# Kernel tuning notes

Measured on AMD Instinct MI355X. Metric: run time of the kernel, lower is better.

The kernel has to match this reference:

```python
import jax, jax.numpy as jnp
import numpy as np

DIM = 2048
BATCH = 16384
NUM_LAYERS = 4
S_E, S_C, S_N = 0.1, 0.1, 0.05  # strength_entail/contra/neutral
DIV_CONST = 0.38                # divergence_from_alignment offset
NORM_CAP = 10.0

def _normalize(x, axis=-1, eps=1e-12):
    # torch F.normalize: x / max(||x||, eps)
    n = jnp.linalg.norm(x, axis=axis, keepdims=True)
    return x / jnp.maximum(n, eps)

def setup_inputs() -> dict:
    key = jax.random.key(0)
    ks = jax.random.split(key, 8)
    scale = 1.0 / np.sqrt(DIM)  # nn.Linear-like init scale
    return {
        "h0": jax.random.normal(ks[0], (BATCH, DIM), dtype=jnp.float32),
        "anchor_entail": jax.random.normal(ks[1], (DIM,), dtype=jnp.float32),
        "anchor_contra": jax.random.normal(ks[2], (DIM,), dtype=jnp.float32),
        "anchor_neutral": jax.random.normal(ks[3], (DIM,), dtype=jnp.float32),
        "W1": jax.random.normal(ks[4], (DIM, DIM), dtype=jnp.float32) * scale,
        "b1": jnp.zeros((DIM,), dtype=jnp.float32),
        "W2": jax.random.normal(ks[5], (DIM, DIM), dtype=jnp.float32) * scale,
        "b2": jnp.zeros((DIM,), dtype=jnp.float32),
    }

def reference(h0, anchor_entail, anchor_contra, anchor_neutral, W1, b1, W2, b2):
    h = h0
    e_dir = _normalize(anchor_entail, axis=0)
    c_dir = _normalize(anchor_contra, axis=0)
    n_dir = _normalize(anchor_neutral, axis=0)
    for _ in range(NUM_LAYERS):
        h_n = _normalize(h)                     # [B, D]
        a_e = h_n @ e_dir                       # [B]
        a_c = h_n @ c_dir
        a_n = h_n @ n_dir
        d_e = DIV_CONST - a_e
        d_c = DIV_CONST - a_c
        d_n = DIV_CONST - a_n
        delta = jnp.tanh(h @ W1.T + b1) @ W2.T + b2  # Linear-Tanh-Linear
        e_vec = _normalize(h - e_dir)
        c_vec = _normalize(h - c_dir)
        n_vec = _normalize(h - n_dir)
        h = (h + delta
             - S_E * d_e[:, None] * e_vec
             - S_C * d_c[:, None] * c_vec
             - S_N * d_n[:, None] * n_vec)
        h_norm = jnp.linalg.norm(h, axis=-1, keepdims=True)
        h = jnp.where(h_norm > NORM_CAP, h * (NORM_CAP / (h_norm + 1e-8)), h)
    return h
```

## Files before the change

### kernel.cpp

```cpp
#include <hip/hip_runtime.h>
#include <stdint.h>

#define DIM      2048
#define BATCH    16384
#define S_E      0.1f
#define S_C      0.1f
#define S_N      0.05f
#define DIVC     0.38f
#define NCAP     10.0f

typedef __attribute__((ext_vector_type(4))) float floatx4;
typedef __attribute__((ext_vector_type(8))) short short8;
typedef __attribute__((ext_vector_type(4))) short short4v;

__device__ __forceinline__ float bf2f(unsigned short u) {
  union { float f; unsigned v; } x; x.v = ((unsigned)u) << 16; return x.f;
}
__device__ __forceinline__ unsigned short f2bf(float f) {
  union { float f; unsigned v; } x; x.f = f;
  unsigned r = x.v + 0x7FFFu + ((x.v >> 16) & 1u);
  return (unsigned short)(r >> 16);
}

__device__ __forceinline__ void gload_lds16(const void* g, void* l) {
  __builtin_amdgcn_global_load_lds((const __attribute__((address_space(1))) void*)g,
                                   (__attribute__((address_space(3))) void*)l,
                                   16, 0, 0);
}

__global__ void k_detect(const unsigned short* __restrict__ h0u, int* __restrict__ flag) {
  const int lane = threadIdx.x;
  int bad = 0;
#pragma unroll
  for (int i = 0; i < 32; ++i) {
    const unsigned u = h0u[lane + i * 64];
    const unsigned e = (u >> 7) & 0xFF;
    bad |= (e >= 0x84);
  }
  const unsigned long long m = __ballot(bad);
  if (lane == 0) *flag = (m != 0ull) ? 1 : 0;
}

__global__ __launch_bounds__(256) void k_prep_w(
    const void* __restrict__ w1r, const void* __restrict__ w2r,
    const int* __restrict__ flag,
    unsigned short* __restrict__ W1b, unsigned short* __restrict__ W2b) {
  const void* src = blockIdx.y ? w2r : w1r;
  unsigned short* dst = blockIdx.y ? W2b : W1b;
  const long i4 = (long)blockIdx.x * 256 + threadIdx.x;
  if (*flag) {
    const float4 v = ((const float4*)src)[i4];
    short4v o;
    o.x = (short)f2bf(v.x); o.y = (short)f2bf(v.y);
    o.z = (short)f2bf(v.z); o.w = (short)f2bf(v.w);
    ((short4v*)dst)[i4] = o;
  } else {
    ((short4v*)dst)[i4] = ((const short4v*)src)[i4];
  }
}

__global__ __launch_bounds__(256) void k_prep_small(
    const void* __restrict__ b1r, const void* __restrict__ b2r,
    const void* __restrict__ a0r, const void* __restrict__ a1r,
    const void* __restrict__ a2r, const int* __restrict__ flag,
    float* __restrict__ b1f, float* __restrict__ b2f, float* __restrict__ dirs) {
  __shared__ float red[4];
  const int tid = threadIdx.x, wave = tid >> 6, lane = tid & 63;
  const int isf32 = *flag;
#pragma unroll
  for (int i = 0; i < 8; ++i) {
    const int idx = i * 256 + tid;
    b1f[idx] = isf32 ? ((const float*)b1r)[idx] : bf2f(((const unsigned short*)b1r)[idx]);
    b2f[idx] = isf32 ? ((const float*)b2r)[idx] : bf2f(((const unsigned short*)b2r)[idx]);
  }
  const void* ar[3] = { a0r, a1r, a2r };
  for (int a = 0; a < 3; ++a) {
    float v[8]; float s = 0.f;
#pragma unroll
    for (int i = 0; i < 8; ++i) {
      const int idx = i * 256 + tid;
      v[i] = isf32 ? ((const float*)ar[a])[idx] : bf2f(((const unsigned short*)ar[a])[idx]);
      s = fmaf(v[i], v[i], s);
    }
#pragma unroll
    for (int off = 32; off >= 1; off >>= 1) s += __shfl_xor(s, off);
    if (lane == 0) red[wave] = s;
    __syncthreads();
    const float S = red[0] + red[1] + red[2] + red[3];
    const float inv = 1.f / fmaxf(sqrtf(S), 1e-12f);
#pragma unroll
    for (int i = 0; i < 8; ++i) dirs[a * DIM + i * 256 + tid] = v[i] * inv;
    __syncthreads();
  }
}

__device__ __forceinline__ float4 row_coef(float S0, float Se, float Sc, float Sn) {
  const float Li = 1.f / fmaxf(sqrtf(S0), 1e-12f);
  const float ce = S_E * (DIVC - Se * Li) / fmaxf(sqrtf(fmaxf(S0 - 2.f * Se + 1.f, 0.f)), 1e-12f);
  const float cc = S_C * (DIVC - Sc * Li) / fmaxf(sqrtf(fmaxf(S0 - 2.f * Sc + 1.f, 0.f)), 1e-12f);
  const float cn = S_N * (DIVC - Sn * Li) / fmaxf(sqrtf(fmaxf(S0 - 2.f * Sn + 1.f, 0.f)), 1e-12f);
  float4 c; c.x = 1.f - (ce + cc + cn); c.y = ce; c.z = cc; c.w = cn; return c;
}

template<int FULL>
__global__ __launch_bounds__(256) void k_boot(
    const void* __restrict__ h0raw, const int* __restrict__ flag,
    const float* __restrict__ dirs, float* __restrict__ hf,
    unsigned short* __restrict__ hb, float4* __restrict__ coef,
    float* __restrict__ scl) {
  __shared__ float red[16];
  const long row = blockIdx.x;
  const int tid = threadIdx.x, wave = tid >> 6, lane = tid & 63;
  const int isf32 = *flag;
  float h[8];
  float s0 = 0.f, se = 0.f, sc = 0.f, sn = 0.f;
#pragma unroll
  for (int i = 0; i < 2; ++i) {
    const int c4 = i * 256 + tid;
    float4 hv;
    if (isf32) {
      hv = ((const float4*)h0raw + row * (DIM/4))[c4];
    } else {
      const short4v hs = ((const short4v*)h0raw + row * (DIM/4))[c4];
      hv.x = bf2f((unsigned short)hs.x); hv.y = bf2f((unsigned short)hs.y);
      hv.z = bf2f((unsigned short)hs.z); hv.w = bf2f((unsigned short)hs.w);
    }
    const float4 ev = ((const float4*)dirs)[c4];
    const float4 cv = ((const float4*)(dirs + DIM))[c4];
    const float4 nv = ((const float4*)(dirs + 2*DIM))[c4];
    h[i*4+0]=hv.x; h[i*4+1]=hv.y; h[i*4+2]=hv.z; h[i*4+3]=hv.w;
    s0 = fmaf(hv.x,hv.x,fmaf(hv.y,hv.y,fmaf(hv.z,hv.z,fmaf(hv.w,hv.w,s0))));
    se = fmaf(hv.x,ev.x,fmaf(hv.y,ev.y,fmaf(hv.z,ev.z,fmaf(hv.w,ev.w,se))));
    sc = fmaf(hv.x,cv.x,fmaf(hv.y,cv.y,fmaf(hv.z,cv.z,fmaf(hv.w,cv.w,sc))));
    sn = fmaf(hv.x,nv.x,fmaf(hv.y,nv.y,fmaf(hv.z,nv.z,fmaf(hv.w,nv.w,sn))));
  }
#pragma unroll
  for (int off = 32; off >= 1; off >>= 1) {
    s0 += __shfl_xor(s0, off); se += __shfl_xor(se, off);
    sc += __shfl_xor(sc, off); sn += __shfl_xor(sn, off);
  }
  if (lane == 0) { red[wave*4+0]=s0; red[wave*4+1]=se; red[wave*4+2]=sc; red[wave*4+3]=sn; }
  __syncthreads();
  if (tid == 0) {
    const float S0 = red[0]+red[4]+red[8]+red[12];
    const float Se = red[1]+red[5]+red[9]+red[13];
    const float Sc = red[2]+red[6]+red[10]+red[14];
    const float Sn = red[3]+red[7]+red[11]+red[15];
    coef[row] = row_coef(S0, Se, Sc, Sn);
    scl[row] = 1.f;
  }
#pragma unroll
  for (int i = 0; i < 2; ++i) {
    const int c4 = i * 256 + tid;
    if (FULL) {
      float4 o; o.x=h[i*4+0]; o.y=h[i*4+1]; o.z=h[i*4+2]; o.w=h[i*4+3];
      ((float4*)hf + row * (DIM/4))[c4] = o;
    }
    short4v ob;
    ob.x=(short)f2bf(h[i*4+0]); ob.y=(short)f2bf(h[i*4+1]);
    ob.z=(short)f2bf(h[i*4+2]); ob.w=(short)f2bf(h[i*4+3]);
    ((short4v*)hb + row * (DIM/4))[c4] = ob;
  }
}


template<int VM, bool STG>
__device__ __forceinline__ void gemm_tile(
    const int t, const unsigned short* __restrict__ Ag,
    const unsigned short* __restrict__ Bg, char* __restrict__ smem,
    const int tid, const int wm, const int wn, const int l16, const int quad,
    floatx4 (&acc)[8][4], short8 (&bfr)[4]) {
  const int qs = (quad ^ ((l16 >> 1) & 3)) * 8;
  const short* As = (const short*)(smem + (t & 3) * 32768) + (wm + l16) * 32 + qs;
  const short* Bs = (const short*)(smem + (t & 3) * 32768 + 16384) + (wn + l16) * 32 + qs;
  short8 af[4];
#pragma unroll
  for (int j = 0; j < 4; ++j) bfr[j] = *(const short8*)(Bs + j * 512);
#pragma unroll
  for (int i = 0; i < 4; ++i) af[i] = *(const short8*)(As + i * 512);
  if (STG) {
    const unsigned short* as = Ag + (t + 3) * 32;
    char* dA = smem + ((t + 3) & 3) * 32768 + tid * 16;
    gload_lds16(as, dA);
    gload_lds16(as + (size_t)128 * DIM, dA + 8192);
  }
  __builtin_amdgcn_s_barrier();
  __builtin_amdgcn_sched_barrier(0);
  __builtin_amdgcn_s_setprio(1);
#pragma unroll
  for (int i = 0; i < 4; ++i)
#pragma unroll
    for (int j = 0; j < 4; ++j)
      acc[i][j] = __builtin_amdgcn_mfma_f32_16x16x32_bf16(af[i], bfr[j], acc[i][j], 0, 0, 0);
  __builtin_amdgcn_s_setprio(0);
  __builtin_amdgcn_s_barrier();
  __builtin_amdgcn_sched_barrier(0);
#pragma unroll
  for (int i = 0; i < 4; ++i) af[i] = *(const short8*)(As + (4 + i) * 512);
  if (STG) {
    const unsigned short* bs = Bg + (t + 3) * 32;
    char* dB = smem + ((t + 3) & 3) * 32768 + 16384 + tid * 16;
    gload_lds16(bs, dB);
    gload_lds16(bs + (size_t)128 * DIM, dB + 8192);
  }
  __builtin_amdgcn_s_barrier();
  __builtin_amdgcn_sched_barrier(0);
  __builtin_amdgcn_s_setprio(1);
#pragma unroll
  for (int i = 0; i < 4; ++i)
#pragma unroll
    for (int j = 0; j < 4; ++j)
      acc[4 + i][j] = __builtin_amdgcn_mfma_f32_16x16x32_bf16(af[i], bfr[j], acc[4 + i][j], 0, 0, 0);
  __builtin_amdgcn_s_setprio(0);
  __builtin_amdgcn_sched_barrier(0);
  if constexpr (VM == 8)      asm volatile("s_waitcnt vmcnt(8)" ::: "memory");
  else if constexpr (VM == 4) asm volatile("s_waitcnt vmcnt(4)" ::: "memory");
  else if constexpr (VM == 0) asm volatile("s_waitcnt vmcnt(0)" ::: "memory");
  __builtin_amdgcn_s_barrier();
  __builtin_amdgcn_sched_barrier(0);
}

__device__ __forceinline__ void gemm_main(
    const unsigned short* __restrict__ A, const unsigned short* __restrict__ B,
    char* __restrict__ smem, const int tid, const int wm, const int wn,
    const int l16, const int quad, const long m0, const long n0,
    floatx4 (&acc)[8][4]) {
  const int csw = ((tid & 3) ^ ((tid >> 3) & 3)) * 8;
  const unsigned short* Ag = A + (m0 + (tid >> 2)) * DIM + csw;
  const unsigned short* Bg = B + (n0 + (tid >> 2)) * DIM + csw;
#pragma unroll
  for (int tt = 0; tt < 3; ++tt) {
    const unsigned short* as = Ag + tt * 32;
    const unsigned short* bs = Bg + tt * 32;
    char* dA = smem + tt * 32768 + tid * 16;
    char* dB = dA + 16384;
    gload_lds16(as, dA);
    gload_lds16(as + (size_t)128 * DIM, dA + 8192);
    gload_lds16(bs, dB);
    gload_lds16(bs + (size_t)128 * DIM, dB + 8192);
  }
  asm volatile("s_waitcnt vmcnt(8)" ::: "memory");
  __builtin_amdgcn_s_barrier();
  __builtin_amdgcn_sched_barrier(0);
  short8 bfr[4];
#pragma unroll 1
  for (int t = 0; t < DIM / 32 - 3; ++t)
    gemm_tile<8, true >(t, Ag, Bg, smem, tid, wm, wn, l16, quad, acc, bfr);
  gemm_tile<4, false>(DIM / 32 - 3, Ag, Bg, smem, tid, wm, wn, l16, quad, acc, bfr);
  gemm_tile<0, false>(DIM / 32 - 2, Ag, Bg, smem, tid, wm, wn, l16, quad, acc, bfr);
  gemm_tile<-1, false>(DIM / 32 - 1, Ag, Bg, smem, tid, wm, wn, l16, quad, acc, bfr);
}

__device__ __forceinline__ void xcd_tiles(long& m0, long& n0) {
  const int b = blockIdx.y * (DIM / 256) + blockIdx.x;
  const int swz = (b & 7) * ((BATCH / 256) * (DIM / 256) / 8) + (b >> 3);
  m0 = (long)(swz >> 3) * 256;
  n0 = (long)(swz & 7) * 256;
}

__global__ __launch_bounds__(512, 2) void gemm_tanh(
    const unsigned short* __restrict__ A, const unsigned short* __restrict__ B,
    const float* __restrict__ bias, const float* __restrict__ scl,
    unsigned short* __restrict__ Cb) {
  __shared__ __align__(16) char smem[131072];
  const int tid = threadIdx.x, wave = tid >> 6, lane = tid & 63;
  const int quad = lane >> 4, l16 = lane & 15;
  const int wm = (wave >> 2) * 128, wn = (wave & 3) * 64;
  long m0, n0;
  xcd_tiles(m0, n0);
  floatx4 acc[8][4] = {};
  gemm_main(A, B, smem, tid, wm, wn, l16, quad, m0, n0, acc);
  __syncthreads();
  asm volatile("" ::: "memory");
  short* Eh = (short*)smem;
  float sr[32];
#pragma unroll
  for (int i = 0; i < 8; ++i) {
    const float4 s4 = *(const float4*)(scl + m0 + wm + i * 16 + quad * 4);
    sr[i*4+0] = s4.x; sr[i*4+1] = s4.y; sr[i*4+2] = s4.z; sr[i*4+3] = s4.w;
  }
  float bcol[4];
#pragma unroll
  for (int j = 0; j < 4; ++j) bcol[j] = bias[n0 + wn + j * 16 + l16];
#pragma unroll
  for (int i = 0; i < 8; ++i) {
    const int row = wm + i * 16 + quad * 4;
#pragma unroll
    for (int j = 0; j < 4; ++j) {
      const int col = wn + j * 16 + l16;
#pragma unroll
      for (int r = 0; r < 4; ++r) {
        const float x = fmaf(sr[i*4+r], acc[i][j][r], bcol[j]);
        const float tt = 1.f - 2.f / (__expf(2.f * x) + 1.f);
        Eh[(row + r) * 256 + col] = (short)f2bf(tt);
      }
    }
  }
  __syncthreads();
#pragma unroll
  for (int s = 0; s < 16; ++s) {
    const int g = s * 512 + tid;
    const int row = g >> 5, c8 = (g & 31) * 8;
    *(short8*)(Cb + (m0 + row) * DIM + n0 + c8) = *(const short8*)(Eh + row * 256 + c8);
  }
}

template<int FULL>
__global__ __launch_bounds__(512, 2) void gemm_update(
    const unsigned short* __restrict__ A, const unsigned short* __restrict__ B,
    const float* __restrict__ bias, float* __restrict__ hf,
    unsigned short* __restrict__ hb, const float4* __restrict__ coef,
    const float* __restrict__ dirs) {
  __shared__ __align__(16) char smem[131072];
  const int tid = threadIdx.x, wave = tid >> 6, lane = tid & 63;
  const int quad = lane >> 4, l16 = lane & 15;
  const int wm = (wave >> 2) * 128, wn = (wave & 3) * 64;
  long m0, n0;
  xcd_tiles(m0, n0);
  floatx4 acc[8][4] = {};
  gemm_main(A, B, smem, tid, wm, wn, l16, quad, m0, n0, acc);
  asm volatile("" ::: "memory");
  float* Ef = (float*)smem;
#pragma unroll
  for (int p = 0; p < 2; ++p) {
    __syncthreads();
#pragma unroll
    for (int i = 0; i < 8; ++i) {
      const int row = wm + i * 16 + quad * 4;
#pragma unroll
      for (int jj = 0; jj < 2; ++jj) {
        const int cc = (wn >> 1) + jj * 16 + l16;
#pragma unroll
        for (int r = 0; r < 4; ++r)
          Ef[(row + r) * 128 + cc] = acc[i][p * 2 + jj][r];
      }
    }
    __syncthreads();
#pragma unroll
    for (int s = 0; s < 16; ++s) {
      const int q = s * 512 + tid;
      const int row = q >> 5, c4 = (q & 31) * 4;
      const int col = ((c4 >> 5) * 64) + p * 32 + (c4 & 31);
      const long gr = m0 + row, gc = n0 + col;
      const float4 e  = *(const float4*)(Ef + row * 128 + c4);
      const float4 bv = *(const float4*)(bias + gc);
      const float4 de = *(const float4*)(dirs + gc);
      const float4 dc = *(const float4*)(dirs + DIM + gc);
      const float4 dn = *(const float4*)(dirs + 2*DIM + gc);
      const float4 cf = coef[gr];
      float4 hv;
      if (FULL) {
        hv = *(const float4*)(hf + gr * DIM + gc);
      } else {
        const short4v hs = *(const short4v*)(hb + gr * DIM + gc);
        hv.x = bf2f((unsigned short)hs.x); hv.y = bf2f((unsigned short)hs.y);
        hv.z = bf2f((unsigned short)hs.z); hv.w = bf2f((unsigned short)hs.w);
      }
      float4 v;
      v.x = e.x + bv.x; v.y = e.y + bv.y; v.z = e.z + bv.z; v.w = e.w + bv.w;
      v.x = fmaf(cf.x, hv.x, v.x); v.y = fmaf(cf.x, hv.y, v.y);
      v.z = fmaf(cf.x, hv.z, v.z); v.w = fmaf(cf.x, hv.w, v.w);
      v.x = fmaf(cf.y, de.x, v.x); v.y = fmaf(cf.y, de.y, v.y);
      v.z = fmaf(cf.y, de.z, v.z); v.w = fmaf(cf.y, de.w, v.w);
      v.x = fmaf(cf.z, dc.x, v.x); v.y = fmaf(cf.z, dc.y, v.y);
      v.z = fmaf(cf.z, dc.z, v.z); v.w = fmaf(cf.z, dc.w, v.w);
      v.x = fmaf(cf.w, dn.x, v.x); v.y = fmaf(cf.w, dn.y, v.y);
      v.z = fmaf(cf.w, dn.z, v.z); v.w = fmaf(cf.w, dn.w, v.w);
      if (FULL) *(float4*)(hf + gr * DIM + gc) = v;
      short4v ob;
      ob.x = (short)f2bf(v.x); ob.y = (short)f2bf(v.y);
      ob.z = (short)f2bf(v.z); ob.w = (short)f2bf(v.w);
      *(short4v*)(hb + gr * DIM + gc) = ob;
    }
  }
}

__global__ __launch_bounds__(256) void k_stats(
    const unsigned short* __restrict__ hb, const float* __restrict__ dirs,
    float4* __restrict__ coef, float* __restrict__ scl) {
  const int tid = threadIdx.x, w = tid >> 6, lane = tid & 63;
  const long row = (long)blockIdx.x * 4 + w;
  const unsigned short* hr = hb + row * DIM;
  float s0 = 0.f, se = 0.f, sc = 0.f, sn = 0.f;
#pragma unroll
  for (int i = 0; i < 4; ++i) {
    const int o = i * 512 + lane * 8;
    const short8 h8 = *(const short8*)(hr + o);
    float h[8];
#pragma unroll
    for (int q = 0; q < 8; ++q) h[q] = bf2f((unsigned short)h8[q]);
    const float4 e0 = *(const float4*)(dirs + o),       e1 = *(const float4*)(dirs + o + 4);
    const float4 c0 = *(const float4*)(dirs + DIM + o), c1 = *(const float4*)(dirs + DIM + o + 4);
    const float4 n0v = *(const float4*)(dirs + 2*DIM + o), n1 = *(const float4*)(dirs + 2*DIM + o + 4);
    const float ee[8] = { e0.x,e0.y,e0.z,e0.w, e1.x,e1.y,e1.z,e1.w };
    const float ccv[8] = { c0.x,c0.y,c0.z,c0.w, c1.x,c1.y,c1.z,c1.w };
    const float nn[8] = { n0v.x,n0v.y,n0v.z,n0v.w, n1.x,n1.y,n1.z,n1.w };
#pragma unroll
    for (int q = 0; q < 8; ++q) {
      s0 = fmaf(h[q], h[q], s0);
      se = fmaf(h[q], ee[q], se);
      sc = fmaf(h[q], ccv[q], sc);
      sn = fmaf(h[q], nn[q], sn);
    }
  }
#pragma unroll
  for (int off = 32; off >= 1; off >>= 1) {
    s0 += __shfl_xor(s0, off); se += __shfl_xor(se, off);
    sc += __shfl_xor(sc, off); sn += __shfl_xor(sn, off);
  }
  if (lane == 0) {
    const float nrm = sqrtf(s0);
    const float s = (nrm > NCAP) ? (NCAP / (nrm + 1e-8f)) : 1.f;
    float4 cf = row_coef(s0 * s * s, se * s, sc * s, sn * s);
    cf.x *= s;
    coef[row] = cf;
    scl[row] = s;
  }
}

template<int FULL>
__global__ __launch_bounds__(256) void k_finish(
    const float* __restrict__ hf, const unsigned short* __restrict__ hb,
    const int* __restrict__ flag, void* __restrict__ dout) {
  const int tid = threadIdx.x, w = tid >> 6, lane = tid & 63;
  const long row = (long)blockIdx.x * 4 + w;
  float4 hv[8];
  float s0 = 0.f;
#pragma unroll
  for (int i = 0; i < 8; ++i) {
    const int o = i * 256 + lane * 4;
    if (FULL) {
      hv[i] = *(const float4*)(hf + row * DIM + o);
    } else {
      const short4v hs = *(const short4v*)(hb + row * DIM + o);
      hv[i].x = bf2f((unsigned short)hs.x); hv[i].y = bf2f((unsigned short)hs.y);
      hv[i].z = bf2f((unsigned short)hs.z); hv[i].w = bf2f((unsigned short)hs.w);
    }
    s0 = fmaf(hv[i].x,hv[i].x,fmaf(hv[i].y,hv[i].y,fmaf(hv[i].z,hv[i].z,fmaf(hv[i].w,hv[i].w,s0))));
  }
#pragma unroll
  for (int off = 32; off >= 1; off >>= 1) s0 += __shfl_xor(s0, off);
  const float nrm = sqrtf(s0);
  const float s = (nrm > NCAP) ? (NCAP / (nrm + 1e-8f)) : 1.f;
  const int isf32 = *flag;
#pragma unroll
  for (int i = 0; i < 8; ++i) {
    const int o = i * 256 + lane * 4;
    float4 v;
    v.x = hv[i].x * s; v.y = hv[i].y * s; v.z = hv[i].z * s; v.w = hv[i].w * s;
    if (isf32) {
      *((float4*)dout + (row * DIM + o) / 4) = v;
    } else {
      short4v ob;
      ob.x = (short)f2bf(v.x); ob.y = (short)f2bf(v.y);
      ob.z = (short)f2bf(v.z); ob.w = (short)f2bf(v.w);
      *((short4v*)dout + (row * DIM + o) / 4) = ob;
    }
  }
}

extern "C" void kernel_launch(void* const* d_in, const int* in_sizes, int n_in,
                              void* d_out, int out_size, void* d_ws, size_t ws_size,
                              hipStream_t stream) {
  const void* h0  = d_in[0];
  const void* A_e = d_in[1];
  const void* A_c = d_in[2];
  const void* A_n = d_in[3];
  const void* W1  = d_in[4];
  const void* b1  = d_in[5];
  const void* W2  = d_in[6];
  const void* b2  = d_in[7];

  char* base = (char*)d_ws;
  size_t off = 0;
  auto take = [&](size_t n) -> char* {
    char* p = base + off; off += (n + 255) & ~(size_t)255; return p;
  };
  int*            flag = (int*)take(4);
  float*          dirs = (float*)take(3 * DIM * 4);
  float*          b1f  = (float*)take(DIM * 4);
  float*          b2f  = (float*)take(DIM * 4);
  float4*         coef = (float4*)take((size_t)BATCH * 16);
  float*          scl  = (float*)take((size_t)BATCH * 4);
  unsigned short* W1b  = (unsigned short*)take((size_t)DIM * DIM * 2);
  unsigned short* W2b  = (unsigned short*)take((size_t)DIM * DIM * 2);
  unsigned short* T    = (unsigned short*)take((size_t)BATCH * DIM * 2);
  unsigned short* hb   = (unsigned short*)take((size_t)BATCH * DIM * 2);
  float*          hf   = (float*)take((size_t)BATCH * DIM * 4);
  const size_t need_full = off;
  const bool full = (ws_size >= need_full);

  k_detect<<<1, 64, 0, stream>>>((const unsigned short*)h0, flag);
  k_prep_w<<<dim3(4096, 2), 256, 0, stream>>>(W1, W2, flag, W1b, W2b);
  k_prep_small<<<1, 256, 0, stream>>>(b1, b2, A_e, A_c, A_n, flag, b1f, b2f, dirs);

  const dim3 gg(DIM / 256, BATCH / 256);
  if (full) {
    k_boot<1><<<BATCH, 256, 0, stream>>>(h0, flag, dirs, hf, hb, coef, scl);
    for (int L = 0; L < 4; ++L) {
      gemm_tanh<<<gg, 512, 0, stream>>>(hb, W1b, b1f, scl, T);
      gemm_update<1><<<gg, 512, 0, stream>>>(T, W2b, b2f, hf, hb, coef, dirs);
      if (L < 3) k_stats<<<BATCH/4, 256, 0, stream>>>(hb, dirs, coef, scl);
    }
    k_finish<1><<<BATCH/4, 256, 0, stream>>>(hf, hb, flag, d_out);
  } else {
    k_boot<0><<<BATCH, 256, 0, stream>>>(h0, flag, dirs, nullptr, hb, coef, scl);
    for (int L = 0; L < 4; ++L) {
      gemm_tanh<<<gg, 512, 0, stream>>>(hb, W1b, b1f, scl, T);
      gemm_update<0><<<gg, 512, 0, stream>>>(T, W2b, b2f, nullptr, hb, coef, dirs);
      if (L < 3) k_stats<<<BATCH/4, 256, 0, stream>>>(hb, dirs, coef, scl);
    }
    k_finish<0><<<BATCH/4, 256, 0, stream>>>(nullptr, hb, flag, d_out);
  }
}
```

Measured before the change: 1.942 ms.

## Restructure GEMM main loop to K=64 double-buffered 8-phase ping-pong schedule

Replaces the 4-stage K=32 LDS ring with a 2-buffer K=64 scheme. Each 64-wide K tile is split into four MFMA phases over A/B halves, with global-to-LDS staging of the next tiles interleaved between phases and an XOR swizzle widened to 8 chunks. The aim is fewer barriers and waits per unit of MFMA work and better overlap of loads with compute. The trade-off is deeper prefetch with clamped redundant loads at the tail, more registers for A fragments, and tighter synchronisation assumptions.

```diff
diff --git a/kernel.cpp b/kernel.cpp
--- a/kernel.cpp
+++ b/kernel.cpp
@@ -164,91 +164,90 @@
 }
 
 
-template<int VM, bool STG>
-__device__ __forceinline__ void gemm_tile(
-    const int t, const unsigned short* __restrict__ Ag,
-    const unsigned short* __restrict__ Bg, char* __restrict__ smem,
-    const int tid, const int wm, const int wn, const int l16, const int quad,
-    floatx4 (&acc)[8][4], short8 (&bfr)[4]) {
-  const int qs = (quad ^ ((l16 >> 1) & 3)) * 8;
-  const short* As = (const short*)(smem + (t & 3) * 32768) + (wm + l16) * 32 + qs;
-  const short* Bs = (const short*)(smem + (t & 3) * 32768 + 16384) + (wn + l16) * 32 + qs;
-  short8 af[4];
-#pragma unroll
-  for (int j = 0; j < 4; ++j) bfr[j] = *(const short8*)(Bs + j * 512);
-#pragma unroll
-  for (int i = 0; i < 4; ++i) af[i] = *(const short8*)(As + i * 512);
-  if (STG) {
-    const unsigned short* as = Ag + (t + 3) * 32;
-    char* dA = smem + ((t + 3) & 3) * 32768 + tid * 16;
-    gload_lds16(as, dA);
-    gload_lds16(as + (size_t)128 * DIM, dA + 8192);
-  }
-  __builtin_amdgcn_s_barrier();
-  __builtin_amdgcn_sched_barrier(0);
-  __builtin_amdgcn_s_setprio(1);
-#pragma unroll
-  for (int i = 0; i < 4; ++i)
-#pragma unroll
-    for (int j = 0; j < 4; ++j)
-      acc[i][j] = __builtin_amdgcn_mfma_f32_16x16x32_bf16(af[i], bfr[j], acc[i][j], 0, 0, 0);
-  __builtin_amdgcn_s_setprio(0);
-  __builtin_amdgcn_s_barrier();
-  __builtin_amdgcn_sched_barrier(0);
-#pragma unroll
-  for (int i = 0; i < 4; ++i) af[i] = *(const short8*)(As + (4 + i) * 512);
-  if (STG) {
-    const unsigned short* bs = Bg + (t + 3) * 32;
-    char* dB = smem + ((t + 3) & 3) * 32768 + 16384 + tid * 16;
-    gload_lds16(bs, dB);
-    gload_lds16(bs + (size_t)128 * DIM, dB + 8192);
-  }
-  __builtin_amdgcn_s_barrier();
-  __builtin_amdgcn_sched_barrier(0);
-  __builtin_amdgcn_s_setprio(1);
-#pragma unroll
-  for (int i = 0; i < 4; ++i)
-#pragma unroll
-    for (int j = 0; j < 4; ++j)
-      acc[4 + i][j] = __builtin_amdgcn_mfma_f32_16x16x32_bf16(af[i], bfr[j], acc[4 + i][j], 0, 0, 0);
-  __builtin_amdgcn_s_setprio(0);
-  __builtin_amdgcn_sched_barrier(0);
-  if constexpr (VM == 8)      asm volatile("s_waitcnt vmcnt(8)" ::: "memory");
-  else if constexpr (VM == 4) asm volatile("s_waitcnt vmcnt(4)" ::: "memory");
-  else if constexpr (VM == 0) asm volatile("s_waitcnt vmcnt(0)" ::: "memory");
-  __builtin_amdgcn_s_barrier();
-  __builtin_amdgcn_sched_barrier(0);
-}
-
 __device__ __forceinline__ void gemm_main(
     const unsigned short* __restrict__ A, const unsigned short* __restrict__ B,
     char* __restrict__ smem, const int tid, const int wm, const int wn,
     const int l16, const int quad, const long m0, const long n0,
     floatx4 (&acc)[8][4]) {
-  const int csw = ((tid & 3) ^ ((tid >> 3) & 3)) * 8;
-  const unsigned short* Ag = A + (m0 + (tid >> 2)) * DIM + csw;
-  const unsigned short* Bg = B + (n0 + (tid >> 2)) * DIM + csw;
-#pragma unroll
-  for (int tt = 0; tt < 3; ++tt) {
-    const unsigned short* as = Ag + tt * 32;
-    const unsigned short* bs = Bg + tt * 32;
-    char* dA = smem + tt * 32768 + tid * 16;
-    char* dB = dA + 16384;
-    gload_lds16(as, dA);
-    gload_lds16(as + (size_t)128 * DIM, dA + 8192);
-    gload_lds16(bs, dB);
-    gload_lds16(bs + (size_t)128 * DIM, dB + 8192);
-  }
-  asm volatile("s_waitcnt vmcnt(8)" ::: "memory");
+  const int s3 = l16 & 7;
+  const int csw = ((tid & 7) ^ ((tid >> 3) & 7)) * 8;
+  const unsigned short* Ag = A + (m0 + (tid >> 3)) * DIM + csw;
+  const unsigned short* Bg = B + (n0 + (tid >> 3)) * DIM + csw;
+  short* lds = (short*)smem;
+  const int ao0 = (wm + l16) * 64 + ((quad ^ s3)) * 8;
+  const int ao1 = (wm + l16) * 64 + (((quad + 4) ^ s3)) * 8;
+  const int bo0 = (wn + l16) * 64 + ((quad ^ s3)) * 8;
+  const int bo1 = (wn + l16) * 64 + (((quad + 4) ^ s3)) * 8;
+
+#define STAGE_A(dbuf, ts, h) { \
+    const unsigned short* s_ = Ag + (size_t)((h) * 128) * DIM + (ts) * 64; \
+    char* d_ = smem + (dbuf) * 65536 + (h) * 16384 + tid * 16; \
+    gload_lds16(s_, d_); gload_lds16(s_ + (size_t)64 * DIM, d_ + 8192); }
+#define STAGE_B(dbuf, ts, h) { \
+    const unsigned short* s_ = Bg + (size_t)((h) * 128) * DIM + (ts) * 64; \
+    char* d_ = smem + (dbuf) * 65536 + 32768 + (h) * 16384 + tid * 16; \
+    gload_lds16(s_, d_); gload_lds16(s_ + (size_t)64 * DIM, d_ + 8192); }
+#define RD_A(dst, bufo, ih) { \
+    _Pragma("unroll") for (int i_ = 0; i_ < 4; ++i_) { \
+      dst[i_][0] = *(const short8*)(lds + (bufo) + (ih) * 4096 + i_ * 1024 + ao0); \
+      dst[i_][1] = *(const short8*)(lds + (bufo) + (ih) * 4096 + i_ * 1024 + ao1); } }
+#define RD_B(bufo, jh) { \
+    _Pragma("unroll") for (int j_ = 0; j_ < 2; ++j_) { \
+      bR[j_][0] = *(const short8*)(lds + (bufo) + 16384 + (jh) * 2048 + j_ * 1024 + bo0); \
+      bR[j_][1] = *(const short8*)(lds + (bufo) + 16384 + (jh) * 2048 + j_ * 1024 + bo1); } }
+#define MF(ih, jh, aR) \
+    __builtin_amdgcn_sched_barrier(0); \
+    __builtin_amdgcn_s_barrier(); \
+    asm volatile("s_waitcnt lgkmcnt(0)" ::: "memory"); \
+    __builtin_amdgcn_sched_barrier(0); \
+    __builtin_amdgcn_s_setprio(1); \
+    _Pragma("unroll") for (int i_ = 0; i_ < 4; ++i_) \
+    _Pragma("unroll") for (int j_ = 0; j_ < 2; ++j_) { \
+      acc[(ih)*4+i_][(jh)*2+j_] = __builtin_amdgcn_mfma_f32_16x16x32_bf16(aR[i_][0], bR[j_][0], acc[(ih)*4+i_][(jh)*2+j_], 0, 0, 0); \
+      acc[(ih)*4+i_][(jh)*2+j_] = __builtin_amdgcn_mfma_f32_16x16x32_bf16(aR[i_][1], bR[j_][1], acc[(ih)*4+i_][(jh)*2+j_], 0, 0, 0); } \
+    __builtin_amdgcn_s_setprio(0); \
+    __builtin_amdgcn_sched_barrier(0);
+#define ENDPH    { __builtin_amdgcn_s_barrier(); __builtin_amdgcn_sched_barrier(0); }
+#define ENDPH_VM { asm volatile("s_waitcnt vmcnt(4)" ::: "memory"); \
+                   __builtin_amdgcn_s_barrier(); __builtin_amdgcn_sched_barrier(0); }
+
+  short8 a0[4][2], a1[4][2], bR[2][2];
+  STAGE_A(0, 0, 0); STAGE_A(0, 0, 1);
+  STAGE_B(0, 0, 0); STAGE_B(0, 0, 1);
+  STAGE_A(1, 1, 0); STAGE_A(1, 1, 1);
+  asm volatile("s_waitcnt vmcnt(4)" ::: "memory");
   __builtin_amdgcn_s_barrier();
   __builtin_amdgcn_sched_barrier(0);
-  short8 bfr[4];
+
 #pragma unroll 1
-  for (int t = 0; t < DIM / 32 - 3; ++t)
-    gemm_tile<8, true >(t, Ag, Bg, smem, tid, wm, wn, l16, quad, acc, bfr);
-  gemm_tile<4, false>(DIM / 32 - 3, Ag, Bg, smem, tid, wm, wn, l16, quad, acc, bfr);
-  gemm_tile<0, false>(DIM / 32 - 2, Ag, Bg, smem, tid, wm, wn, l16, quad, acc, bfr);
-  gemm_tile<-1, false>(DIM / 32 - 1, Ag, Bg, smem, tid, wm, wn, l16, quad, acc, bfr);
+  for (int it = 0; it < DIM / 128; ++it) {
+    const int t = it * 2;
+    const int t2 = (t + 2 < 31) ? (t + 2) : 31;
+    const int t3 = (t + 3 < 31) ? (t + 3) : 31;
+    RD_A(a0, 0, 0); RD_B(0, 0); STAGE_B(1, t + 1, 0);
+    MF(0, 0, a0) ENDPH
+    RD_A(a1, 0, 1); STAGE_B(1, t + 1, 1);
+    MF(1, 0, a1) ENDPH
+    RD_B(0, 1); STAGE_A(0, t2, 0);
+    MF(0, 1, a0) ENDPH
+    STAGE_A(0, t2, 1);
+    MF(1, 1, a1) ENDPH_VM
+    RD_A(a0, 32768, 0); RD_B(32768, 0); STAGE_B(0, t2, 0);
+    MF(0, 0, a0) ENDPH
+    RD_A(a1, 32768, 1); STAGE_B(0, t2, 1);
+    MF(1, 0, a1) ENDPH
+    RD_B(32768, 1); STAGE_A(1, t3, 0);
+    MF(0, 1, a0) ENDPH
+    STAGE_A(1, t3, 1);
+    MF(1, 1, a1) ENDPH_VM
+  }
+#undef STAGE_A
+#undef STAGE_B
+#undef RD_A
+#undef RD_B
+#undef MF
+#undef ENDPH
+#undef ENDPH_VM
 }
 
 __device__ __forceinline__ void xcd_tiles(long& m0, long& n0) {
```

After: 1.864 ms. 1.04x faster.
